# Performance work log

Measured on AMD Instinct MI355X. Metric: run time of the kernel, lower is better.

The kernel has to match this reference:

```python
import jax, jax.numpy as jnp
import numpy as np

B, T, D = 32, 4096, 128

def setup_inputs() -> dict:
    key = jax.random.key(0)
    k1, k2, k3 = jax.random.split(key, 3)
    values = jax.random.normal(k1, (B, T, D), dtype=jnp.float32)
    # monotonically increasing observation times per (batch, channel)
    dt = jax.random.uniform(k2, (B, T, D), dtype=jnp.float32, minval=0.1, maxval=1.0)
    times = jnp.cumsum(dt, axis=1)
    mask = jax.random.bernoulli(k3, 0.5, (B, T, D))  # True = observed
    return {"values": values, "times": times, "mask": mask}


def _carry_fill(values, times, mask):
    """Last/next-observed fill via log-depth cummax/cummin on indices (replaces
    the per-timestep keras RNN tf.where loop)."""
    ar = jnp.arange(T, dtype=jnp.int32)[None, :, None]
    # ---- forward: last observed value/time (inclusive of current step) ----
    idx_f = jnp.where(mask, ar, jnp.int32(-1))
    last_idx = jax.lax.cummax(idx_f, axis=1)
    has_last = last_idx >= 0
    gi = jnp.clip(last_idx, 0, T - 1)
    x_last = jnp.where(has_last, jnp.take_along_axis(values, gi, axis=1), 0.0)
    # initial forward state: x=0, t=times[:,0,:]
    t_last = jnp.where(has_last, jnp.take_along_axis(times, gi, axis=1), times[:, :1, :])
    # ---- backward: next observed value/time (inclusive of current step) ----
    idx_b = jnp.where(mask, ar, jnp.int32(T))
    next_idx = jnp.flip(jax.lax.cummin(jnp.flip(idx_b, axis=1), axis=1), axis=1)
    has_next = next_idx < T
    gj = jnp.clip(next_idx, 0, T - 1)
    x_next = jnp.where(has_next, jnp.take_along_axis(values, gj, axis=1), 0.0)
    # initial backward state: x=0, t=max(times) over time
    t_max = jnp.max(times, axis=1, keepdims=True)
    t_next = jnp.where(has_next, jnp.take_along_axis(times, gj, axis=1), t_max)
    return x_last, t_last, x_next, t_next


def reference(values, times, mask):
    x_last, t_last, x_next, t_next = _carry_fill(values, times, mask)
    denom = t_next - t_last
    valid = denom != 0  # nan/inf from zero-length interval -> 0, as in tf code
    num = x_last * (t_next - times) + x_next * (times - t_last)
    x_itp = jnp.where(valid, num / jnp.where(valid, denom, 1.0), 0.0)
    return jnp.where(mask, values, x_itp)
```

## Files before the change

### kernel.cpp

```cpp
#include <hip/hip_runtime.h>
#include <hip/hip_bf16.h>

#define Bq 32
#define Tq 4096
#define Dq 128
#define Lseg 32
#define NSEG (Tq / Lseg)
#define SRCH 8

__device__ __forceinline__ float bfbits2f(unsigned short u) {
    return __uint_as_float(((unsigned int)u) << 16);
}
__device__ __forceinline__ unsigned short f2hbits(float x) {
    union { _Float16 h; unsigned short s; } cv;
    cv.h = (_Float16)x;
    return cv.s;
}
__device__ __forceinline__ float hbits2f(unsigned short u) {
    union { unsigned short s; _Float16 h; } cv;
    cv.s = u;
    return (float)cv.h;
}
__device__ __forceinline__ float ldval(const void* p, int idx, int f32) {
    if (f32) return ((const float*)p)[idx];
    return bfbits2f(((const unsigned short*)p)[idx]);
}
__device__ __forceinline__ bool ldmask(const void* p, int idx, int mode) {
    switch (mode) {
        case 1:  return ((const int*)p)[idx] != 0;
        case 2:  return ((const unsigned short*)p)[idx] != 0;
        case 3:  return ((const unsigned int*)p)[idx] != 0;
        default: return ((const unsigned char*)p)[idx] != 0;
    }
}

#define DECLQ(q) float tmL_##q, tmH_##q; unsigned int pnx_##q, pdt_##q;

#define BHI(q) { \
    const int rr = 2*(q) + 1; \
    const int idx = base + (sLo + rr) * Dq; \
    float v  = ldval(values, idx, f32); \
    float tm = ldval(times,  idx, f32); \
    bool  m  = ldmask(mask,  idx, mmode); \
    if (m) { bx = v; bt = tm; mbits |= (1u << rr); } \
    tmH_##q = tm; \
    pnx_##q = ((unsigned int)f2hbits(bx)) << 16; \
    pdt_##q = ((unsigned int)f2hbits(bt - tm)) << 16; }

#define BLO(q) { \
    const int rr = 2*(q); \
    const int idx = base + (sLo + rr) * Dq; \
    float v  = ldval(values, idx, f32); \
    float tm = ldval(times,  idx, f32); \
    bool  m  = ldmask(mask,  idx, mmode); \
    if (m) { bx = v; bt = tm; mbits |= (1u << rr); } \
    tmL_##q = tm; \
    pnx_##q |= (unsigned int)f2hbits(bx); \
    pdt_##q |= (unsigned int)f2hbits(bt - tm); }

#define FEMIT(rr, tm, dtn, nx) { \
    bool m = (mbits >> (rr)) & 1u; \
    float ox; \
    if (m) { fx = (nx); ft = (tm); ox = (nx); } \
    else { \
        float a = (tm) - ft; \
        float denom = (dtn) + a; \
        float num = fx * (dtn) + (nx) * a; \
        ox = (denom != 0.f) ? (num / denom) : 0.f; \
    } \
    out[base + (sLo + (rr)) * Dq] = ox; }

#define FLO(q) { \
    float tm  = tmL_##q; \
    float dtn = hbits2f((unsigned short)(pdt_##q & 0xFFFFu)); \
    float nx  = hbits2f((unsigned short)(pnx_##q & 0xFFFFu)); \
    FEMIT(2*(q), tm, dtn, nx) }

#define FHI(q) { \
    float tm  = tmH_##q; \
    float dtn = hbits2f((unsigned short)(pdt_##q >> 16)); \
    float nx  = hbits2f((unsigned short)(pnx_##q >> 16)); \
    FEMIT(2*(q)+1, tm, dtn, nx) }

#define BPROBE(j) \
    int bm##j; float bv##j, btm##j; { \
        int rj = r + (j); int rc = rj < Tq ? rj : Tq - 1; \
        int idx = base + rc * Dq; \
        bm##j  = (int)ldmask(mask, idx, mmode) & (int)(rj < Tq); \
        bv##j  = ldval(values, idx, f32); \
        btm##j = ldval(times,  idx, f32); }
#define BSEL(j) if (!found && bm##j) { bx = bv##j; bt = btm##j; found = 1; }

#define FPROBE(j) \
    int fm##j; float fv##j, ftm##j; { \
        int rj = r - (j); int rc = rj > 0 ? rj : 0; \
        int idx = base + rc * Dq; \
        fm##j  = (int)ldmask(mask, idx, mmode) & (int)(rj >= 0); \
        fv##j  = ldval(values, idx, f32); \
        ftm##j = ldval(times,  idx, f32); }
#define FSEL(j) if (!found && fm##j) { fx = fv##j; ft = ftm##j; found = 1; }

__global__ __launch_bounds__(128, 3) void interp_kernel(
    const void* __restrict__ values,
    const void* __restrict__ times,
    const void* __restrict__ mask,
    float* __restrict__ out)
{
    const int lane = threadIdx.x & 63;

    int mmode, f32;
    {
        const unsigned int* mu = (const unsigned int*)mask;
        int bad_f32 = 0, bad_b16 = 0, off_nz = 0;
        for (int j = lane; j < 1024; j += 64) {
            unsigned int w = mu[j];
            if (w != 0u && w != 0x3F800000u) bad_f32 = 1;
            unsigned int h0 = w & 0xFFFFu, h1 = w >> 16;
            if ((h0 != 0u && h0 != 0x3F80u) || (h1 != 0u && h1 != 0x3F80u)) bad_b16 = 1;
            if (w & 0xFFFFFF00u) off_nz = 1;
        }
        if      (__ballot(bad_f32) == 0ull) mmode = 3;
        else if (__ballot(bad_b16) == 0ull) mmode = 2;
        else if (__ballot(off_nz)  == 0ull) mmode = 1;
        else                                mmode = 0;

        const unsigned short* tu = (const unsigned short*)times;
        int good = 0;
        for (int k = lane; k < 256; k += 64) {
            int ex = (tu[2 * k] >> 7) & 0xFF;
            if (ex >= 118 && ex <= 142) good++;
        }
        for (int off = 32; off; off >>= 1) good += __shfl_xor(good, off, 64);
        f32 = (good < 128) ? 1 : 0;
    }

    const int b   = blockIdx.x >> 7;
    const int s   = blockIdx.x & (NSEG - 1);
    const int d   = threadIdx.x;
    const int sLo = s * Lseg;
    const int sHi = sLo + Lseg;
    const int base = b * Tq * Dq + d;

    float bx = 0.f, bt = 0.f;
    {
        int found = 0;
        for (int r = sHi; r < Tq; r += SRCH) {
            if (__ballot(!found) == 0ull) break;
            BPROBE(0) BPROBE(1) BPROBE(2) BPROBE(3)
            BPROBE(4) BPROBE(5) BPROBE(6) BPROBE(7)
            BSEL(0) BSEL(1) BSEL(2) BSEL(3)
            BSEL(4) BSEL(5) BSEL(6) BSEL(7)
        }
        if (!found) bt = ldval(times, base + (Tq - 1) * Dq, f32);
    }

    float fx = 0.f, ft = 0.f;
    {
        int found = 0;
        for (int r = sLo - 1; r >= 0; r -= SRCH) {
            if (__ballot(!found) == 0ull) break;
            FPROBE(0) FPROBE(1) FPROBE(2) FPROBE(3)
            FPROBE(4) FPROBE(5) FPROBE(6) FPROBE(7)
            FSEL(0) FSEL(1) FSEL(2) FSEL(3)
            FSEL(4) FSEL(5) FSEL(6) FSEL(7)
        }
        if (!found) ft = ldval(times, base, f32);
    }

    DECLQ(0)  DECLQ(1)  DECLQ(2)  DECLQ(3)
    DECLQ(4)  DECLQ(5)  DECLQ(6)  DECLQ(7)
    DECLQ(8)  DECLQ(9)  DECLQ(10) DECLQ(11)
    DECLQ(12) DECLQ(13) DECLQ(14) DECLQ(15)
    unsigned int mbits = 0;

    BHI(15) BLO(15) BHI(14) BLO(14) BHI(13) BLO(13) BHI(12) BLO(12)
    BHI(11) BLO(11) BHI(10) BLO(10) BHI(9)  BLO(9)  BHI(8)  BLO(8)
    BHI(7)  BLO(7)  BHI(6)  BLO(6)  BHI(5)  BLO(5)  BHI(4)  BLO(4)
    BHI(3)  BLO(3)  BHI(2)  BLO(2)  BHI(1)  BLO(1)  BHI(0)  BLO(0)

    FLO(0)  FHI(0)  FLO(1)  FHI(1)  FLO(2)  FHI(2)  FLO(3)  FHI(3)
    FLO(4)  FHI(4)  FLO(5)  FHI(5)  FLO(6)  FHI(6)  FLO(7)  FHI(7)
    FLO(8)  FHI(8)  FLO(9)  FHI(9)  FLO(10) FHI(10) FLO(11) FHI(11)
    FLO(12) FHI(12) FLO(13) FHI(13) FLO(14) FHI(14) FLO(15) FHI(15)
}

extern "C" void kernel_launch(void* const* d_in, const int* in_sizes, int n_in,
                              void* d_out, int out_size, void* d_ws, size_t ws_size,
                              hipStream_t stream) {
    const void* values = d_in[0];
    const void* times  = d_in[1];
    const void* mask   = d_in[2];
    float* out = (float*)d_out;
    (void)d_ws; (void)ws_size;

    interp_kernel<<<Bq * NSEG, 128, 0, stream>>>(values, times, mask, out);
}
```

Baseline: 314.3 us.

## Split boundary search into separate kernel writing carry state to workspace

```diff
diff --git a/kernel.cpp b/kernel.cpp
--- a/kernel.cpp
+++ b/kernel.cpp
@@ -6,7 +6,10 @@
 #define Dq 128
 #define Lseg 32
 #define NSEG (Tq / Lseg)
+#define NBLK (Bq * NSEG)
 #define SRCH 8
+#define NSITE (Bq * NSEG * Dq)
+#define WS_NEED (6u * 1024u * 1024u)
 
 __device__ __forceinline__ float bfbits2f(unsigned short u) {
     return __uint_as_float(((unsigned int)u) << 16);
@@ -33,6 +36,50 @@
         default: return ((const unsigned char*)p)[idx] != 0;
     }
 }
+
+__device__ __forceinline__ void detect_dtypes(const void* mask, const void* times,
+                                              int lane, int& mmode, int& f32) {
+    const unsigned int* mu = (const unsigned int*)mask;
+    int bad_f32 = 0, bad_b16 = 0, off_nz = 0;
+    for (int j = lane; j < 1024; j += 64) {
+        unsigned int w = mu[j];
+        if (w != 0u && w != 0x3F800000u) bad_f32 = 1;
+        unsigned int h0 = w & 0xFFFFu, h1 = w >> 16;
+        if ((h0 != 0u && h0 != 0x3F80u) || (h1 != 0u && h1 != 0x3F80u)) bad_b16 = 1;
+        if (w & 0xFFFFFF00u) off_nz = 1;
+    }
+    if      (__ballot(bad_f32) == 0ull) mmode = 3;
+    else if (__ballot(bad_b16) == 0ull) mmode = 2;
+    else if (__ballot(off_nz)  == 0ull) mmode = 1;
+    else                                mmode = 0;
+
+    const unsigned short* tu = (const unsigned short*)times;
+    int good = 0;
+    for (int k = lane; k < 256; k += 64) {
+        int ex = (tu[2 * k] >> 7) & 0xFF;
+        if (ex >= 118 && ex <= 142) good++;
+    }
+    for (int off = 32; off; off >>= 1) good += __shfl_xor(good, off, 64);
+    f32 = (good < 128) ? 1 : 0;
+}
+
+#define BPROBE(j) \
+    int bm##j; float bv##j, btm##j; { \
+        int rj = r + (j); int rc = rj < Tq ? rj : Tq - 1; \
+        int idx = base + rc * Dq; \
+        bm##j  = (int)ldmask(mask, idx, mmode) & (int)(rj < Tq); \
+        bv##j  = ldval(values, idx, f32); \
+        btm##j = ldval(times,  idx, f32); }
+#define BSEL(j) if (!found && bm##j) { bx = bv##j; bt = btm##j; found = 1; }
+
+#define FPROBE(j) \
+    int fm##j; float fv##j, ftm##j; { \
+        int rj = r - (j); int rc = rj > 0 ? rj : 0; \
+        int idx = base + rc * Dq; \
+        fm##j  = (int)ldmask(mask, idx, mmode) & (int)(rj >= 0); \
+        fv##j  = ldval(values, idx, f32); \
+        ftm##j = ldval(times,  idx, f32); }
+#define FSEL(j) if (!found && fm##j) { fx = fv##j; ft = ftm##j; found = 1; }
 
 #define DECLQ(q) float tmL_##q, tmH_##q; unsigned int pnx_##q, pdt_##q;
 
@@ -82,57 +129,105 @@
     float nx  = hbits2f((unsigned short)(pnx_##q >> 16)); \
     FEMIT(2*(q)+1, tm, dtn, nx) }
 
-#define BPROBE(j) \
-    int bm##j; float bv##j, btm##j; { \
-        int rj = r + (j); int rc = rj < Tq ? rj : Tq - 1; \
-        int idx = base + rc * Dq; \
-        bm##j  = (int)ldmask(mask, idx, mmode) & (int)(rj < Tq); \
-        bv##j  = ldval(values, idx, f32); \
-        btm##j = ldval(times,  idx, f32); }
-#define BSEL(j) if (!found && bm##j) { bx = bv##j; bt = btm##j; found = 1; }
-
-#define FPROBE(j) \
-    int fm##j; float fv##j, ftm##j; { \
-        int rj = r - (j); int rc = rj > 0 ? rj : 0; \
-        int idx = base + rc * Dq; \
-        fm##j  = (int)ldmask(mask, idx, mmode) & (int)(rj >= 0); \
-        fv##j  = ldval(values, idx, f32); \
-        ftm##j = ldval(times,  idx, f32); }
-#define FSEL(j) if (!found && fm##j) { fx = fv##j; ft = ftm##j; found = 1; }
-
-__global__ __launch_bounds__(128, 3) void interp_kernel(
+#define BSEARCH_BODY { \
+    int found = 0; \
+    for (int r = sHi; r < Tq; r += SRCH) { \
+        if (__ballot(!found) == 0ull) break; \
+        BPROBE(0) BPROBE(1) BPROBE(2) BPROBE(3) \
+        BPROBE(4) BPROBE(5) BPROBE(6) BPROBE(7) \
+        BSEL(0) BSEL(1) BSEL(2) BSEL(3) \
+        BSEL(4) BSEL(5) BSEL(6) BSEL(7) \
+    } \
+    if (!found) bt = ldval(times, base + (Tq - 1) * Dq, f32); }
+
+#define FSEARCH_BODY { \
+    int found = 0; \
+    for (int r = sLo - 1; r >= 0; r -= SRCH) { \
+        if (__ballot(!found) == 0ull) break; \
+        FPROBE(0) FPROBE(1) FPROBE(2) FPROBE(3) \
+        FPROBE(4) FPROBE(5) FPROBE(6) FPROBE(7) \
+        FSEL(0) FSEL(1) FSEL(2) FSEL(3) \
+        FSEL(4) FSEL(5) FSEL(6) FSEL(7) \
+    } \
+    if (!found) ft = ldval(times, base, f32); }
+
+#define SWEEP_AND_EMIT_BODY { \
+    DECLQ(0)  DECLQ(1)  DECLQ(2)  DECLQ(3) \
+    DECLQ(4)  DECLQ(5)  DECLQ(6)  DECLQ(7) \
+    DECLQ(8)  DECLQ(9)  DECLQ(10) DECLQ(11) \
+    DECLQ(12) DECLQ(13) DECLQ(14) DECLQ(15) \
+    unsigned int mbits = 0; \
+    BHI(15) BLO(15) BHI(14) BLO(14) BHI(13) BLO(13) BHI(12) BLO(12) \
+    BHI(11) BLO(11) BHI(10) BLO(10) BHI(9)  BLO(9)  BHI(8)  BLO(8)  \
+    BHI(7)  BLO(7)  BHI(6)  BLO(6)  BHI(5)  BLO(5)  BHI(4)  BLO(4)  \
+    BHI(3)  BLO(3)  BHI(2)  BLO(2)  BHI(1)  BLO(1)  BHI(0)  BLO(0)  \
+    FLO(0)  FHI(0)  FLO(1)  FHI(1)  FLO(2)  FHI(2)  FLO(3)  FHI(3)  \
+    FLO(4)  FHI(4)  FLO(5)  FHI(5)  FLO(6)  FHI(6)  FLO(7)  FHI(7)  \
+    FLO(8)  FHI(8)  FLO(9)  FHI(9)  FLO(10) FHI(10) FLO(11) FHI(11) \
+    FLO(12) FHI(12) FLO(13) FHI(13) FLO(14) FHI(14) FLO(15) FHI(15) }
+
+__global__ __launch_bounds__(128) void search_kernel(
+    const void* __restrict__ values,
+    const void* __restrict__ times,
+    const void* __restrict__ mask,
+    unsigned short* __restrict__ fxa, float* __restrict__ fta,
+    unsigned short* __restrict__ bxa, float* __restrict__ bta)
+{
+    const int lane = threadIdx.x & 63;
+    int mmode, f32;
+    detect_dtypes(mask, times, lane, mmode, f32);
+
+    const int b   = blockIdx.x >> 7;
+    const int s   = blockIdx.x & (NSEG - 1);
+    const int d   = threadIdx.x;
+    const int sLo = s * Lseg;
+    const int sHi = sLo + Lseg;
+    const int base = b * Tq * Dq + d;
+
+    float bx = 0.f, bt = 0.f;
+    BSEARCH_BODY
+    float fx = 0.f, ft = 0.f;
+    FSEARCH_BODY
+
+    const int si = blockIdx.x * Dq + d;
+    fxa[si] = f2hbits(fx);  fta[si] = ft;
+    bxa[si] = f2hbits(bx);  bta[si] = bt;
+}
+
+__global__ __launch_bounds__(128, 3) void main_kernel(
+    const void* __restrict__ values,
+    const void* __restrict__ times,
+    const void* __restrict__ mask,
+    float* __restrict__ out,
+    const unsigned short* __restrict__ fxa, const float* __restrict__ fta,
+    const unsigned short* __restrict__ bxa, const float* __restrict__ bta)
+{
+    const int lane = threadIdx.x & 63;
+    int mmode, f32;
+    detect_dtypes(mask, times, lane, mmode, f32);
+
+    const int b   = blockIdx.x >> 7;
+    const int s   = blockIdx.x & (NSEG - 1);
+    const int d   = threadIdx.x;
+    const int sLo = s * Lseg;
+    const int base = b * Tq * Dq + d;
+
+    const int si = blockIdx.x * Dq + d;
+    float fx = hbits2f(fxa[si]);  float ft = fta[si];
+    float bx = hbits2f(bxa[si]);  float bt = bta[si];
+
+    SWEEP_AND_EMIT_BODY
+}
+
+__global__ __launch_bounds__(128, 3) void interp_fallback(
     const void* __restrict__ values,
     const void* __restrict__ times,
     const void* __restrict__ mask,
     float* __restrict__ out)
 {
     const int lane = threadIdx.x & 63;
-
     int mmode, f32;
-    {
-        const unsigned int* mu = (const unsigned int*)mask;
-        int bad_f32 = 0, bad_b16 = 0, off_nz = 0;
-        for (int j = lane; j < 1024; j += 64) {
-            unsigned int w = mu[j];
-            if (w != 0u && w != 0x3F800000u) bad_f32 = 1;
-            unsigned int h0 = w & 0xFFFFu, h1 = w >> 16;
-            if ((h0 != 0u && h0 != 0x3F80u) || (h1 != 0u && h1 != 0x3F80u)) bad_b16 = 1;
-            if (w & 0xFFFFFF00u) off_nz = 1;
-        }
-        if      (__ballot(bad_f32) == 0ull) mmode = 3;
-        else if (__ballot(bad_b16) == 0ull) mmode = 2;
-        else if (__ballot(off_nz)  == 0ull) mmode = 1;
-        else                                mmode = 0;
-
-        const unsigned short* tu = (const unsigned short*)times;
-        int good = 0;
-        for (int k = lane; k < 256; k += 64) {
-            int ex = (tu[2 * k] >> 7) & 0xFF;
-            if (ex >= 118 && ex <= 142) good++;
-        }
-        for (int off = 32; off; off >>= 1) good += __shfl_xor(good, off, 64);
-        f32 = (good < 128) ? 1 : 0;
-    }
+    detect_dtypes(mask, times, lane, mmode, f32);
 
     const int b   = blockIdx.x >> 7;
     const int s   = blockIdx.x & (NSEG - 1);
@@ -142,46 +237,11 @@
     const int base = b * Tq * Dq + d;
 
     float bx = 0.f, bt = 0.f;
-    {
-        int found = 0;
-        for (int r = sHi; r < Tq; r += SRCH) {
-            if (__ballot(!found) == 0ull) break;
-            BPROBE(0) BPROBE(1) BPROBE(2) BPROBE(3)
-            BPROBE(4) BPROBE(5) BPROBE(6) BPROBE(7)
-            BSEL(0) BSEL(1) BSEL(2) BSEL(3)
-            BSEL(4) BSEL(5) BSEL(6) BSEL(7)
-        }
-        if (!found) bt = ldval(times, base + (Tq - 1) * Dq, f32);
-    }
-
+    BSEARCH_BODY
     float fx = 0.f, ft = 0.f;
-    {
-        int found = 0;
-        for (int r = sLo - 1; r >= 0; r -= SRCH) {
-            if (__ballot(!found) == 0ull) break;
-            FPROBE(0) FPROBE(1) FPROBE(2) FPROBE(3)
-            FPROBE(4) FPROBE(5) FPROBE(6) FPROBE(7)
-            FSEL(0) FSEL(1) FSEL(2) FSEL(3)
-            FSEL(4) FSEL(5) FSEL(6) FSEL(7)
-        }
-        if (!found) ft = ldval(times, base, f32);
-    }
-
-    DECLQ(0)  DECLQ(1)  DECLQ(2)  DECLQ(3)
-    DECLQ(4)  DECLQ(5)  DECLQ(6)  DECLQ(7)
-    DECLQ(8)  DECLQ(9)  DECLQ(10) DECLQ(11)
-    DECLQ(12) DECLQ(13) DECLQ(14) DECLQ(15)
-    unsigned int mbits = 0;
-
-    BHI(15) BLO(15) BHI(14) BLO(14) BHI(13) BLO(13) BHI(12) BLO(12)
-    BHI(11) BLO(11) BHI(10) BLO(10) BHI(9)  BLO(9)  BHI(8)  BLO(8)
-    BHI(7)  BLO(7)  BHI(6)  BLO(6)  BHI(5)  BLO(5)  BHI(4)  BLO(4)
-    BHI(3)  BLO(3)  BHI(2)  BLO(2)  BHI(1)  BLO(1)  BHI(0)  BLO(0)
-
-    FLO(0)  FHI(0)  FLO(1)  FHI(1)  FLO(2)  FHI(2)  FLO(3)  FHI(3)
-    FLO(4)  FHI(4)  FLO(5)  FHI(5)  FLO(6)  FHI(6)  FLO(7)  FHI(7)
-    FLO(8)  FHI(8)  FLO(9)  FHI(9)  FLO(10) FHI(10) FLO(11) FHI(11)
-    FLO(12) FHI(12) FLO(13) FHI(13) FLO(14) FHI(14) FLO(15) FHI(15)
+    FSEARCH_BODY
+
+    SWEEP_AND_EMIT_BODY
 }
 
 extern "C" void kernel_launch(void* const* d_in, const int* in_sizes, int n_in,
@@ -191,7 +251,18 @@
     const void* times  = d_in[1];
     const void* mask   = d_in[2];
     float* out = (float*)d_out;
-    (void)d_ws; (void)ws_size;
-
-    interp_kernel<<<Bq * NSEG, 128, 0, stream>>>(values, times, mask, out);
-}
+
+    if (d_ws != nullptr && ws_size >= WS_NEED) {
+        char* w = (char*)d_ws;
+        unsigned short* fxa = (unsigned short*)(w);
+        unsigned short* bxa = (unsigned short*)(w + 1u*1024u*1024u);
+        float*          fta = (float*)(w + 2u*1024u*1024u);
+        float*          bta = (float*)(w + 4u*1024u*1024u);
+        search_kernel<<<NBLK, 128, 0, stream>>>(values, times, mask,
+                                                fxa, fta, bxa, bta);
+        main_kernel<<<NBLK, 128, 0, stream>>>(values, times, mask, out,
+                                              fxa, fta, bxa, bta);
+    } else {
+        interp_fallback<<<NBLK, 128, 0, stream>>>(values, times, mask, out);
+    }
+}
```

New measurement: 305.0 us. -3.0%, faster.
